# Optimization experiments

Hardware: AMD Instinct MI355X
Metric: run time of the kernel (lower is better)

## Reference

```python
import jax, jax.numpy as jnp
import numpy as np

ALPHA = 1.0 / 10.0  # dt / tau

def setup_inputs() -> dict:
    key = jax.random.key(0)
    ks = jax.random.split(key, 5)
    seq_len, batch, input_dim, hidden = 256, 128, 256, 1024
    return {
        "input": jax.random.normal(ks[0], (seq_len, batch, input_dim), dtype=jnp.float32),
        "W_in": jax.random.normal(ks[1], (hidden, input_dim), dtype=jnp.float32) / np.sqrt(input_dim),
        "b_in": jax.random.normal(ks[2], (hidden,), dtype=jnp.float32) * 0.01,
        "W_hh": jax.random.normal(ks[3], (hidden, hidden), dtype=jnp.float32) / np.sqrt(hidden),
        "b_hh": jax.random.normal(ks[4], (hidden,), dtype=jnp.float32) * 0.01,
        "h0": jnp.zeros((hidden,), dtype=jnp.float32),
    }

def reference(input, W_in, b_in, W_hh, b_hh, h0):
    # input: [T, B, I] -> states: [T, B, H]
    # Precompute input projections for all timesteps (linear, same math as per-step).
    x_proj = jnp.einsum('tbi,hi->tbh', input, W_in) + b_in  # [T, B, H]
    h_init = jnp.broadcast_to(h0, (input.shape[1], h0.shape[0]))  # [B, H]

    def step(h, xp):
        rec = h @ W_hh.T + b_hh                       # [B, H]
        h_new = (1.0 - ALPHA) * h + ALPHA * (rec + xp)  # leaky integration (noise sigma = 0)
        h_new = jax.nn.relu(h_new)
        return h_new, h_new

    _, states = jax.lax.scan(step, h_init, x_proj)
    return states  # [T, B, H]
```

## Files before the change

kernel.cpp:

```cpp
#include <hip/hip_runtime.h>
#include <hip/hip_bf16.h>

#define T_LEN 256
#define B_DIM 128
#define I_DIM 256
#define H_DIM 1024

typedef __attribute__((ext_vector_type(8))) short short8;
typedef __attribute__((ext_vector_type(4))) float f32x4;

__device__ unsigned g_sync[256];

static __device__ __forceinline__ unsigned short f2bf(float f) {
  unsigned u = __float_as_uint(f);
  return (unsigned short)((u + 0x7fffu + ((u >> 16) & 1u)) >> 16);
}
static __device__ __forceinline__ float bf2f(unsigned short h) {
  return __uint_as_float((unsigned)h << 16);
}

__global__ __launch_bounds__(256) void xproj_gemm(
    const float* __restrict__ A, const float* __restrict__ W,
    const float* __restrict__ bias, float* __restrict__ C) {
  __shared__ float As[64][33];
  __shared__ float Ws[64][33];

  const int tid = threadIdx.x;
  const int m0 = blockIdx.y * 64;
  const int n0 = blockIdx.x * 64;
  const int ty = tid >> 4;
  const int tx = tid & 15;
  const int r   = tid >> 3;
  const int c4  = (tid & 7) << 2;

  float acc[4][4] = {};

  for (int kc = 0; kc < I_DIM; kc += 32) {
#pragma unroll
    for (int p = 0; p < 2; ++p) {
      const int rr = r + p * 32;
      const float4 a = *(const float4*)(A + (size_t)(m0 + rr) * I_DIM + kc + c4);
      As[rr][c4 + 0] = a.x; As[rr][c4 + 1] = a.y;
      As[rr][c4 + 2] = a.z; As[rr][c4 + 3] = a.w;
      const float4 w = *(const float4*)(W + (size_t)(n0 + rr) * I_DIM + kc + c4);
      Ws[rr][c4 + 0] = w.x; Ws[rr][c4 + 1] = w.y;
      Ws[rr][c4 + 2] = w.z; Ws[rr][c4 + 3] = w.w;
    }
    __syncthreads();
#pragma unroll
    for (int k = 0; k < 32; ++k) {
      float av[4], wv[4];
#pragma unroll
      for (int i = 0; i < 4; ++i) av[i] = As[ty * 4 + i][k];
#pragma unroll
      for (int j = 0; j < 4; ++j) wv[j] = Ws[tx * 4 + j][k];
#pragma unroll
      for (int i = 0; i < 4; ++i)
#pragma unroll
        for (int j = 0; j < 4; ++j)
          acc[i][j] = fmaf(av[i], wv[j], acc[i][j]);
    }
    __syncthreads();
  }

  const float4 bv = *(const float4*)(bias + n0 + tx * 4);
#pragma unroll
  for (int i = 0; i < 4; ++i) {
    float4 o;
    o.x = acc[i][0] + bv.x;
    o.y = acc[i][1] + bv.y;
    o.z = acc[i][2] + bv.z;
    o.w = acc[i][3] + bv.w;
    *(float4*)(C + (size_t)(m0 + ty * 4 + i) * H_DIM + n0 + tx * 4) = o;
  }
}

__global__ __launch_bounds__(256) void cvt_hi_lo(
    const float* __restrict__ X, unsigned short* __restrict__ Xh,
    unsigned short* __restrict__ Xl) {
  const int i4 = blockIdx.x * 256 + threadIdx.x;
  const float4 x = ((const float4*)X)[i4];
  ushort4 h, l;
  h.x = f2bf(x.x); l.x = f2bf(x.x - bf2f(h.x));
  h.y = f2bf(x.y); l.y = f2bf(x.y - bf2f(h.y));
  h.z = f2bf(x.z); l.z = f2bf(x.z - bf2f(h.z));
  h.w = f2bf(x.w); l.w = f2bf(x.w - bf2f(h.w));
  ((ushort4*)Xh)[i4] = h;
  ((ushort4*)Xl)[i4] = l;
}

__global__ __launch_bounds__(256) void xproj_mfma(
    const unsigned short* __restrict__ Ah, const unsigned short* __restrict__ Al,
    const unsigned short* __restrict__ Wh, const unsigned short* __restrict__ Wl,
    const float* __restrict__ bias, float* __restrict__ C) {
  const int tid  = threadIdx.x;
  const int wv   = tid >> 6;
  const int lane = tid & 63;
  const int ln   = lane & 15;
  const int q    = lane >> 4;
  const int mw   = wv >> 1;
  const int nw   = wv & 1;
  const int m0   = blockIdx.y * 128 + mw * 64;
  const int n0   = blockIdx.x * 64  + nw * 32;

  f32x4 acc[4][2] = {};

#pragma unroll
  for (int kc = 0; kc < 8; ++kc) {
    const int ko = kc * 32 + q * 8;
    short8 afh[4], afl[4], wfh[2], wfl[2];
#pragma unroll
    for (int fm = 0; fm < 4; ++fm) {
      const size_t off = (size_t)(m0 + fm * 16 + ln) * I_DIM + ko;
      afh[fm] = *(const short8*)(Ah + off);
      afl[fm] = *(const short8*)(Al + off);
    }
#pragma unroll
    for (int fn = 0; fn < 2; ++fn) {
      const size_t off = (size_t)(n0 + fn * 16 + ln) * I_DIM + ko;
      wfh[fn] = *(const short8*)(Wh + off);
      wfl[fn] = *(const short8*)(Wl + off);
    }
#pragma unroll
    for (int fm = 0; fm < 4; ++fm)
#pragma unroll
      for (int fn = 0; fn < 2; ++fn) {
        acc[fm][fn] = __builtin_amdgcn_mfma_f32_16x16x32_bf16(afh[fm], wfh[fn], acc[fm][fn], 0, 0, 0);
        acc[fm][fn] = __builtin_amdgcn_mfma_f32_16x16x32_bf16(afh[fm], wfl[fn], acc[fm][fn], 0, 0, 0);
        acc[fm][fn] = __builtin_amdgcn_mfma_f32_16x16x32_bf16(afl[fm], wfh[fn], acc[fm][fn], 0, 0, 0);
      }
  }

#pragma unroll
  for (int fn = 0; fn < 2; ++fn) {
    const int j = n0 + fn * 16 + ln;
    const float bj = bias[j];
#pragma unroll
    for (int fm = 0; fm < 4; ++fm)
#pragma unroll
      for (int r = 0; r < 4; ++r)
        C[(size_t)(m0 + fm * 16 + q * 4 + r) * H_DIM + j] = acc[fm][fn][r] + bj;
  }
}

__global__ __launch_bounds__(256) void cvt_w_bf16(
    const float* __restrict__ W, unsigned short* __restrict__ Wb) {
  const int i4 = blockIdx.x * 256 + threadIdx.x;
  const float4 w = ((const float4*)W)[i4];
  ushort4 o;
  o.x = f2bf(w.x); o.y = f2bf(w.y); o.z = f2bf(w.z); o.w = f2bf(w.w);
  ((ushort4*)Wb)[i4] = o;
}

__global__ __launch_bounds__(256) void init_hT0(
    const float* __restrict__ h0, unsigned short* __restrict__ hT) {
  const int idx = blockIdx.x * 256 + threadIdx.x;
  hT[idx] = f2bf(h0[idx & (H_DIM - 1)]);
  if (blockIdx.x == 0) g_sync[threadIdx.x] = 0u;
}

__global__ __launch_bounds__(256, 1) void rnn_persist(
    unsigned short* __restrict__ hT,
    const unsigned short* __restrict__ Wb,
    const float* __restrict__ b_hh,
    const float* __restrict__ h0,
    float* __restrict__ out)
{
  __shared__ float red[2][16][33];

  const int tid  = threadIdx.x;
  const int wv   = tid >> 6;
  const int lane = tid & 63;
  const int ln   = lane & 15;
  const int q    = lane >> 4;

  const int bid = blockIdx.x;
  const int bq  = bid >> 5;
  const int lj  = bid & 31;
  const int j0  = lj * 32;
  const int mt  = wv & 1;
  const int kh  = wv >> 1;
  const int b0  = bq * 32 + mt * 16;

  short8 wfrag[2][16];
#pragma unroll
  for (int jf = 0; jf < 2; ++jf) {
    const short8* __restrict__ wb8 =
        (const short8*)(Wb + (size_t)(j0 + jf * 16 + ln) * H_DIM + kh * 512 + q * 8);
#pragma unroll
    for (int kc = 0; kc < 16; ++kc) wfrag[jf][kc] = wb8[kc * 4];
  }

  const size_t HT = (size_t)B_DIM * H_DIM;
  const size_t arow = (size_t)(b0 + ln) * H_DIM + kh * 512 + q * 8;
  const unsigned short* __restrict__ ha0 = hT + arow;
  const unsigned short* __restrict__ ha1 = hT + HT + arow;

  float bj[2];
#pragma unroll
  for (int jf = 0; jf < 2; ++jf) bj[jf] = b_hh[j0 + jf * 16 + ln];

  const size_t obase = (size_t)(b0 + q * 4) * H_DIM + j0 + ln;

  float hcur[2][4];
#pragma unroll
  for (int jf = 0; jf < 2; ++jf) {
    const float h0j = h0[j0 + jf * 16 + ln];
#pragma unroll
    for (int r = 0; r < 4; ++r) hcur[jf][r] = h0j;
  }

  unsigned* flags = &g_sync[bq * 32];
  unsigned* myflag = &g_sync[bq * 32 + lj];
  unsigned* pollp  = &g_sync[bq * 32 + kh * 16 + ln];

  for (int t = 0; t < T_LEN; ++t) {
#pragma unroll
    for (int jf = 0; jf < 2; ++jf)
#pragma unroll
      for (int kc = 0; kc < 16; ++kc) asm volatile("" : "+v"(wfrag[jf][kc]));

    float* __restrict__ xio_t = out + (size_t)t * HT;

    float xpv[2][4];
    if (wv < 2) {
#pragma unroll
      for (int jf = 0; jf < 2; ++jf)
#pragma unroll
        for (int r = 0; r < 4; ++r)
          xpv[jf][r] = xio_t[obase + (size_t)r * H_DIM + jf * 16];
    }

    if (t > 0) {
      const unsigned tgt = (unsigned)t;
      for (;;) {
        unsigned fv;
        asm volatile("global_load_dword %0, %1, off sc0 sc1\n\t"
                     "s_waitcnt vmcnt(0)"
                     : "=v"(fv) : "v"(pollp) : "memory");
        if (__all((int)fv >= (int)tgt)) break;
        __builtin_amdgcn_s_sleep(1);
      }
    }
    __builtin_amdgcn_sched_barrier(0);

    const unsigned short* __restrict__ ha = (t & 1) ? ha1 : ha0;
    short8 hfrag[16];
#pragma unroll
    for (int kc = 0; kc < 16; ++kc) {
      asm volatile("global_load_dwordx4 %0, %1, off offset:%2 sc0 sc1"
                   : "=&v"(hfrag[kc]) : "v"(ha), "i"(kc * 64));
    }
    asm volatile("s_waitcnt vmcnt(0)" ::: "memory");
    __builtin_amdgcn_sched_barrier(0);

    f32x4 a0[2], a1[2];
#pragma unroll
    for (int jf = 0; jf < 2; ++jf) { a0[jf] = (f32x4){0,0,0,0}; a1[jf] = (f32x4){0,0,0,0}; }
#pragma unroll
    for (int kc = 0; kc < 16; kc += 2) {
#pragma unroll
      for (int jf = 0; jf < 2; ++jf) {
        a0[jf] = __builtin_amdgcn_mfma_f32_16x16x32_bf16(hfrag[kc],     wfrag[jf][kc],     a0[jf], 0, 0, 0);
        a1[jf] = __builtin_amdgcn_mfma_f32_16x16x32_bf16(hfrag[kc + 1], wfrag[jf][kc + 1], a1[jf], 0, 0, 0);
      }
    }
    f32x4 acc[2];
#pragma unroll
    for (int jf = 0; jf < 2; ++jf) acc[jf] = a0[jf] + a1[jf];

    if (wv >= 2) {
#pragma unroll
      for (int jf = 0; jf < 2; ++jf)
#pragma unroll
        for (int r = 0; r < 4; ++r) red[mt][q * 4 + r][jf * 16 + ln] = acc[jf][r];
    }
    __syncthreads();
    if (wv < 2) {
      unsigned short* __restrict__ hnext = hT + (size_t)((t + 1) & 1) * HT;
#pragma unroll
      for (int jf = 0; jf < 2; ++jf)
#pragma unroll
        for (int r = 0; r < 4; ++r) {
          const float rec = acc[jf][r] + red[mt][q * 4 + r][jf * 16 + ln];
          float v = 0.9f * hcur[jf][r] + 0.1f * (rec + bj[jf] + xpv[jf][r]);
          v = v > 0.f ? v : 0.f;
          hcur[jf][r] = v;
          const size_t oidx = obase + (size_t)r * H_DIM + jf * 16;
          xio_t[oidx] = v;
          __hip_atomic_store(&hnext[oidx], f2bf(v), __ATOMIC_RELAXED,
                             __HIP_MEMORY_SCOPE_AGENT);
        }
    }
    __syncthreads();
    if (tid == 0)
      __hip_atomic_store(myflag, (unsigned)(t + 1), __ATOMIC_RELAXED,
                         __HIP_MEMORY_SCOPE_AGENT);
  }
  (void)flags;
}

extern "C" void kernel_launch(void* const* d_in, const int* in_sizes, int n_in,
                              void* d_out, int out_size, void* d_ws, size_t ws_size,
                              hipStream_t stream) {
  const float* input = (const float*)d_in[0];
  const float* W_in  = (const float*)d_in[1];
  const float* b_in  = (const float*)d_in[2];
  const float* W_hh  = (const float*)d_in[3];
  const float* b_hh  = (const float*)d_in[4];
  const float* h0    = (const float*)d_in[5];
  float* out = (float*)d_out;

  char* ws = (char*)d_ws;
  unsigned short* Wb  = (unsigned short*)ws;
  unsigned short* hT  = (unsigned short*)(ws + (2u << 20));
  unsigned short* Wih = (unsigned short*)(ws + (5u << 19));
  unsigned short* Wil = (unsigned short*)(ws + (3u << 20));
  unsigned short* Ah  = (unsigned short*)(ws + (4u << 20));
  unsigned short* Al  = (unsigned short*)(ws + (20u << 20));

  cvt_w_bf16<<<(H_DIM * H_DIM / 4) / 256, 256, 0, stream>>>(W_hh, Wb);
  init_hT0<<<(B_DIM * H_DIM) / 256, 256, 0, stream>>>(h0, hT);

  if (ws_size >= (36u << 20)) {
    cvt_hi_lo<<<(T_LEN * B_DIM * I_DIM / 4) / 256, 256, 0, stream>>>(input, Ah, Al);
    cvt_hi_lo<<<(H_DIM * I_DIM / 4) / 256, 256, 0, stream>>>(W_in, Wih, Wil);
    dim3 g1(H_DIM / 64, (T_LEN * B_DIM) / 128);
    xproj_mfma<<<g1, 256, 0, stream>>>(Ah, Al, Wih, Wil, b_in, out);
  } else {
    dim3 g1(H_DIM / 64, (T_LEN * B_DIM) / 64);
    xproj_gemm<<<g1, 256, 0, stream>>>(input, W_in, b_in, out);
  }

  {
    unsigned short* hT_ = hT;
    const unsigned short* Wb_ = Wb;
    const float* bhh_ = b_hh;
    const float* h0_ = h0;
    float* out_ = out;
    void* pargs[5] = {(void*)&hT_, (void*)&Wb_, (void*)&bhh_, (void*)&h0_, (void*)&out_};
    hipLaunchCooperativeKernel((const void*)rnn_persist, dim3(128), dim3(256),
                               pargs, 0, stream);
  }
}
```

Baseline: 1.552 ms.

## Move W_hh fragments to LDS, prefetch next x-proj, and per-wave flag signalling

Weight fragments move from VGPRs into shared memory and are read from LDS inside the MFMA loop, which lowers register pressure at the cost of extra LDS traffic every step. The next timestep's input projection is prefetched while the current h loads are in flight. The reduction buffer is double-buffered so the second __syncthreads can be dropped. Each writer wave now publishes its own flag right after its h stores, with the output store moved after the flag, so the next step's dependency is released sooner. The change depends on the relaxed stores and vmcnt waits being enough to order the h writes before the flag.

After: 1.936 ms. +24.7%, slower.

```diff
diff --git a/kernel.cpp b/kernel.cpp
--- a/kernel.cpp
+++ b/kernel.cpp
@@ -166,7 +166,8 @@
     const float* __restrict__ h0,
     float* __restrict__ out)
 {
-  __shared__ float red[2][16][33];
+  __shared__ short8 w_lds[2 * 2 * 16 * 64];
+  __shared__ float red[2][2][16][33];
 
   const int tid  = threadIdx.x;
   const int wv   = tid >> 6;
@@ -182,13 +183,13 @@
   const int kh  = wv >> 1;
   const int b0  = bq * 32 + mt * 16;
 
-  short8 wfrag[2][16];
-#pragma unroll
-  for (int jf = 0; jf < 2; ++jf) {
-    const short8* __restrict__ wb8 =
-        (const short8*)(Wb + (size_t)(j0 + jf * 16 + ln) * H_DIM + kh * 512 + q * 8);
-#pragma unroll
-    for (int kc = 0; kc < 16; ++kc) wfrag[jf][kc] = wb8[kc * 4];
+  {
+    const int kh_f = wv >> 1, jf_f = wv & 1;
+    const short8* __restrict__ src =
+        (const short8*)(Wb + (size_t)(j0 + jf_f * 16 + ln) * H_DIM + kh_f * 512 + q * 8);
+    short8* dst = &w_lds[((kh_f * 2 + jf_f) * 16) * 64 + lane];
+#pragma unroll
+    for (int kc = 0; kc < 16; ++kc) dst[kc * 64] = src[kc * 4];
   }
 
   const size_t HT = (size_t)B_DIM * H_DIM;
@@ -210,27 +211,21 @@
     for (int r = 0; r < 4; ++r) hcur[jf][r] = h0j;
   }
 
-  unsigned* flags = &g_sync[bq * 32];
-  unsigned* myflag = &g_sync[bq * 32 + lj];
-  unsigned* pollp  = &g_sync[bq * 32 + kh * 16 + ln];
+  unsigned* pollp  = &g_sync[bq * 64 + kh * 32 + ((lane & 15) << 1) + mt];
+  unsigned* myflag = &g_sync[bq * 64 + (lj << 1) + mt];
+
+  float xcur[2][4];
+  if (wv < 2) {
+#pragma unroll
+    for (int jf = 0; jf < 2; ++jf)
+#pragma unroll
+      for (int r = 0; r < 4; ++r)
+        xcur[jf][r] = out[obase + (size_t)r * H_DIM + jf * 16];
+  }
+  asm volatile("s_waitcnt vmcnt(0)" ::: "memory");
+  __syncthreads();
 
   for (int t = 0; t < T_LEN; ++t) {
-#pragma unroll
-    for (int jf = 0; jf < 2; ++jf)
-#pragma unroll
-      for (int kc = 0; kc < 16; ++kc) asm volatile("" : "+v"(wfrag[jf][kc]));
-
-    float* __restrict__ xio_t = out + (size_t)t * HT;
-
-    float xpv[2][4];
-    if (wv < 2) {
-#pragma unroll
-      for (int jf = 0; jf < 2; ++jf)
-#pragma unroll
-        for (int r = 0; r < 4; ++r)
-          xpv[jf][r] = xio_t[obase + (size_t)r * H_DIM + jf * 16];
-    }
-
     if (t > 0) {
       const unsigned tgt = (unsigned)t;
       for (;;) {
@@ -239,7 +234,7 @@
                      "s_waitcnt vmcnt(0)"
                      : "=v"(fv) : "v"(pollp) : "memory");
         if (__all((int)fv >= (int)tgt)) break;
-        __builtin_amdgcn_s_sleep(1);
+        __builtin_amdgcn_s_sleep(2);
       }
     }
     __builtin_amdgcn_sched_barrier(0);
@@ -251,7 +246,23 @@
       asm volatile("global_load_dwordx4 %0, %1, off offset:%2 sc0 sc1"
                    : "=&v"(hfrag[kc]) : "v"(ha), "i"(kc * 64));
     }
-    asm volatile("s_waitcnt vmcnt(0)" ::: "memory");
+
+    float xnext[2][4];
+    if (wv < 2) {
+      const int tn = (t + 1 < T_LEN) ? t + 1 : T_LEN - 1;
+      const float* __restrict__ xnp = out + (size_t)tn * HT;
+#pragma unroll
+      for (int jf = 0; jf < 2; ++jf)
+#pragma unroll
+        for (int r = 0; r < 4; ++r) {
+          const float* p = xnp + obase + (size_t)r * H_DIM + jf * 16;
+          asm volatile("global_load_dword %0, %1, off"
+                       : "=&v"(xnext[jf][r]) : "v"(p));
+        }
+      asm volatile("s_waitcnt vmcnt(8)" ::: "memory");
+    } else {
+      asm volatile("s_waitcnt vmcnt(0)" ::: "memory");
+    }
     __builtin_amdgcn_sched_barrier(0);
 
     f32x4 a0[2], a1[2];
@@ -261,8 +272,10 @@
     for (int kc = 0; kc < 16; kc += 2) {
 #pragma unroll
       for (int jf = 0; jf < 2; ++jf) {
-        a0[jf] = __builtin_amdgcn_mfma_f32_16x16x32_bf16(hfrag[kc],     wfrag[jf][kc],     a0[jf], 0, 0, 0);
-        a1[jf] = __builtin_amdgcn_mfma_f32_16x16x32_bf16(hfrag[kc + 1], wfrag[jf][kc + 1], a1[jf], 0, 0, 0);
+        const short8 w0 = w_lds[((kh * 2 + jf) * 16 + kc) * 64 + lane];
+        const short8 w1 = w_lds[((kh * 2 + jf) * 16 + kc + 1) * 64 + lane];
+        a0[jf] = __builtin_amdgcn_mfma_f32_16x16x32_bf16(hfrag[kc],     w0, a0[jf], 0, 0, 0);
+        a1[jf] = __builtin_amdgcn_mfma_f32_16x16x32_bf16(hfrag[kc + 1], w1, a1[jf], 0, 0, 0);
       }
     }
     f32x4 acc[2];
@@ -273,31 +286,42 @@
 #pragma unroll
       for (int jf = 0; jf < 2; ++jf)
 #pragma unroll
-        for (int r = 0; r < 4; ++r) red[mt][q * 4 + r][jf * 16 + ln] = acc[jf][r];
+        for (int r = 0; r < 4; ++r)
+          red[t & 1][mt][q * 4 + r][jf * 16 + ln] = acc[jf][r];
     }
     __syncthreads();
     if (wv < 2) {
       unsigned short* __restrict__ hnext = hT + (size_t)((t + 1) & 1) * HT;
+      float* __restrict__ xio_t = out + (size_t)t * HT;
+      float v[2][4];
 #pragma unroll
       for (int jf = 0; jf < 2; ++jf)
 #pragma unroll
         for (int r = 0; r < 4; ++r) {
-          const float rec = acc[jf][r] + red[mt][q * 4 + r][jf * 16 + ln];
-          float v = 0.9f * hcur[jf][r] + 0.1f * (rec + bj[jf] + xpv[jf][r]);
-          v = v > 0.f ? v : 0.f;
-          hcur[jf][r] = v;
-          const size_t oidx = obase + (size_t)r * H_DIM + jf * 16;
-          xio_t[oidx] = v;
-          __hip_atomic_store(&hnext[oidx], f2bf(v), __ATOMIC_RELAXED,
-                             __HIP_MEMORY_SCOPE_AGENT);
+          const float rec = acc[jf][r] + red[t & 1][mt][q * 4 + r][jf * 16 + ln];
+          float x = 0.9f * hcur[jf][r] + 0.1f * (rec + bj[jf] + xcur[jf][r]);
+          x = x > 0.f ? x : 0.f;
+          v[jf][r] = x;
+          hcur[jf][r] = x;
+          __hip_atomic_store(&hnext[obase + (size_t)r * H_DIM + jf * 16],
+                             f2bf(x), __ATOMIC_RELAXED, __HIP_MEMORY_SCOPE_AGENT);
         }
-    }
-    __syncthreads();
-    if (tid == 0)
-      __hip_atomic_store(myflag, (unsigned)(t + 1), __ATOMIC_RELAXED,
-                         __HIP_MEMORY_SCOPE_AGENT);
-  }
-  (void)flags;
+      asm volatile("s_waitcnt vmcnt(0)" ::: "memory");
+      __builtin_amdgcn_sched_barrier(0);
+      if ((tid & 63) == 0)
+        __hip_atomic_store(myflag, (unsigned)(t + 1), __ATOMIC_RELAXED,
+                           __HIP_MEMORY_SCOPE_AGENT);
+#pragma unroll
+      for (int jf = 0; jf < 2; ++jf)
+#pragma unroll
+        for (int r = 0; r < 4; ++r)
+          xio_t[obase + (size_t)r * H_DIM + jf * 16] = v[jf][r];
+#pragma unroll
+      for (int jf = 0; jf < 2; ++jf)
+#pragma unroll
+        for (int r = 0; r < 4; ++r) xcur[jf][r] = xnext[jf][r];
+    }
+  }
 }
 
 extern "C" void kernel_launch(void* const* d_in, const int* in_sizes, int n_in,
```

## Shrink persistent RNN to 32 blocks with wider column tiles and L2-streamed weights

Applied to the files above, without the earlier changes.

The recurrent persistent kernel moves from 128 blocks of 256 threads to 32 blocks of 512 threads. Each block now covers 128 hidden columns and splits K four ways across warps, reducing partials through shared memory. Weights are no longer held in registers but reloaded from global memory (L2) each step. The flag poll moves to the end of the step and the next x-projection is prefetched in the epilogue, so fewer blocks synchronise and wait latency is hidden. The cost is using far fewer CUs and extra weight traffic per step.

Measured after the change: 5.474 ms. 253% more time.

```diff
diff --git a/kernel.cpp b/kernel.cpp
--- a/kernel.cpp
+++ b/kernel.cpp
@@ -159,14 +159,14 @@
   if (blockIdx.x == 0) g_sync[threadIdx.x] = 0u;
 }
 
-__global__ __launch_bounds__(256, 1) void rnn_persist(
+__global__ __launch_bounds__(512, 1) void rnn_persist(
     unsigned short* __restrict__ hT,
     const unsigned short* __restrict__ Wb,
     const float* __restrict__ b_hh,
     const float* __restrict__ h0,
     float* __restrict__ out)
 {
-  __shared__ float red[2][16][33];
+  __shared__ float red[2][3][16][132];
 
   const int tid  = threadIdx.x;
   const int wv   = tid >> 6;
@@ -175,129 +175,122 @@
   const int q    = lane >> 4;
 
   const int bid = blockIdx.x;
-  const int bq  = bid >> 5;
-  const int lj  = bid & 31;
-  const int j0  = lj * 32;
+  const int bq  = bid >> 3;
+  const int lj  = bid & 7;
+  const int j0  = lj * 128;
   const int mt  = wv & 1;
-  const int kh  = wv >> 1;
+  const int kq  = wv >> 1;
   const int b0  = bq * 32 + mt * 16;
 
-  short8 wfrag[2][16];
-#pragma unroll
-  for (int jf = 0; jf < 2; ++jf) {
-    const short8* __restrict__ wb8 =
-        (const short8*)(Wb + (size_t)(j0 + jf * 16 + ln) * H_DIM + kh * 512 + q * 8);
-#pragma unroll
-    for (int kc = 0; kc < 16; ++kc) wfrag[jf][kc] = wb8[kc * 4];
-  }
-
   const size_t HT = (size_t)B_DIM * H_DIM;
-  const size_t arow = (size_t)(b0 + ln) * H_DIM + kh * 512 + q * 8;
-  const unsigned short* __restrict__ ha0 = hT + arow;
-  const unsigned short* __restrict__ ha1 = hT + HT + arow;
-
-  float bj[2];
-#pragma unroll
-  for (int jf = 0; jf < 2; ++jf) bj[jf] = b_hh[j0 + jf * 16 + ln];
-
-  const size_t obase = (size_t)(b0 + q * 4) * H_DIM + j0 + ln;
-
-  float hcur[2][4];
-#pragma unroll
-  for (int jf = 0; jf < 2; ++jf) {
-    const float h0j = h0[j0 + jf * 16 + ln];
-#pragma unroll
-    for (int r = 0; r < 4; ++r) hcur[jf][r] = h0j;
-  }
-
-  unsigned* flags = &g_sync[bq * 32];
-  unsigned* myflag = &g_sync[bq * 32 + lj];
-  unsigned* pollp  = &g_sync[bq * 32 + kh * 16 + ln];
+  const unsigned short* __restrict__ ha0 =
+      hT + (size_t)(b0 + ln) * H_DIM + kq * 256 + q * 8;
+  const unsigned short* __restrict__ ha1 = ha0 + HT;
+  const unsigned short* __restrict__ wbase0 =
+      Wb + (size_t)(j0 + ln) * H_DIM + kq * 256 + q * 8;
+
+  const bool epi = (kq == 0);
+
+  float bj[8], hcur[8][4], xcur[8][4];
+  if (epi) {
+#pragma unroll
+    for (int jf = 0; jf < 8; ++jf) {
+      bj[jf] = b_hh[j0 + jf * 16 + ln];
+      const float h0j = h0[j0 + jf * 16 + ln];
+#pragma unroll
+      for (int r = 0; r < 4; ++r) {
+        hcur[jf][r] = h0j;
+        xcur[jf][r] = out[(size_t)(b0 + q * 4 + r) * H_DIM + j0 + jf * 16 + ln];
+      }
+    }
+  }
+
+  unsigned* myflag = &g_sync[bq * 16 + lj * 2 + mt];
+  unsigned* pollw  = &g_sync[bq * 16 + ln];
 
   for (int t = 0; t < T_LEN; ++t) {
-#pragma unroll
-    for (int jf = 0; jf < 2; ++jf)
-#pragma unroll
-      for (int kc = 0; kc < 16; ++kc) asm volatile("" : "+v"(wfrag[jf][kc]));
-
-    float* __restrict__ xio_t = out + (size_t)t * HT;
-
-    float xpv[2][4];
-    if (wv < 2) {
-#pragma unroll
-      for (int jf = 0; jf < 2; ++jf)
+    __syncthreads();
+
+    const unsigned short* wb = wbase0;
+    asm volatile("" : "+v"(wb));
+
+    const unsigned short* __restrict__ ha = (t & 1) ? ha1 : ha0;
+    short8 hfrag[8];
+#pragma unroll
+    for (int kc = 0; kc < 8; ++kc) {
+      asm volatile("global_load_dwordx4 %0, %1, off offset:%2 sc0 sc1"
+                   : "=&v"(hfrag[kc]) : "v"(ha), "i"(kc * 64));
+    }
+    asm volatile("s_waitcnt vmcnt(0)" ::: "memory");
+    __builtin_amdgcn_sched_barrier(0);
+
+    f32x4 acc[8];
+#pragma unroll
+    for (int jf = 0; jf < 8; ++jf) acc[jf] = (f32x4){0.f, 0.f, 0.f, 0.f};
+#pragma unroll
+    for (int kc = 0; kc < 8; ++kc) {
+#pragma unroll
+      for (int jf = 0; jf < 8; ++jf) {
+        const short8 wf = *(const short8*)(wb + (size_t)jf * 16 * H_DIM + kc * 32);
+        acc[jf] = __builtin_amdgcn_mfma_f32_16x16x32_bf16(hfrag[kc], wf, acc[jf], 0, 0, 0);
+      }
+    }
+
+    if (!epi) {
+#pragma unroll
+      for (int jf = 0; jf < 8; ++jf)
 #pragma unroll
         for (int r = 0; r < 4; ++r)
-          xpv[jf][r] = xio_t[obase + (size_t)r * H_DIM + jf * 16];
-    }
-
-    if (t > 0) {
-      const unsigned tgt = (unsigned)t;
+          red[mt][kq - 1][q * 4 + r][jf * 16 + ln] = acc[jf][r];
+    }
+    __syncthreads();
+
+    if (epi) {
+      unsigned short* __restrict__ hnext = hT + (size_t)((t + 1) & 1) * HT;
+      float* __restrict__ xio_t = out + (size_t)t * HT;
+      float v[8][4];
+#pragma unroll
+      for (int jf = 0; jf < 8; ++jf)
+#pragma unroll
+        for (int r = 0; r < 4; ++r) {
+          const int jl = jf * 16 + ln;
+          const int bl = q * 4 + r;
+          const float rec = acc[jf][r] + red[mt][0][bl][jl] +
+                            red[mt][1][bl][jl] + red[mt][2][bl][jl];
+          float x = 0.9f * hcur[jf][r] + 0.1f * (rec + bj[jf] + xcur[jf][r]);
+          x = x > 0.f ? x : 0.f;
+          v[jf][r] = x;
+          hcur[jf][r] = x;
+          __hip_atomic_store(&hnext[(size_t)(b0 + bl) * H_DIM + j0 + jl],
+                             f2bf(x), __ATOMIC_RELAXED, __HIP_MEMORY_SCOPE_AGENT);
+        }
+      asm volatile("s_waitcnt vmcnt(0)" ::: "memory");
+      __builtin_amdgcn_sched_barrier(0);
+      if (lane == 0)
+        __hip_atomic_store(myflag, (unsigned)(t + 1), __ATOMIC_RELAXED,
+                           __HIP_MEMORY_SCOPE_AGENT);
+      const int tn = (t + 1 < T_LEN) ? t + 1 : t;
+      const float* __restrict__ xnp = out + (size_t)tn * HT;
+#pragma unroll
+      for (int jf = 0; jf < 8; ++jf)
+#pragma unroll
+        for (int r = 0; r < 4; ++r) {
+          const size_t oidx = (size_t)(b0 + q * 4 + r) * H_DIM + j0 + jf * 16 + ln;
+          xio_t[oidx] = v[jf][r];
+          xcur[jf][r] = xnp[oidx];
+        }
+    } else if (wv == 2 && t + 1 < T_LEN) {
+      const unsigned tgt = (unsigned)(t + 1);
       for (;;) {
         unsigned fv;
         asm volatile("global_load_dword %0, %1, off sc0 sc1\n\t"
                      "s_waitcnt vmcnt(0)"
-                     : "=v"(fv) : "v"(pollp) : "memory");
+                     : "=v"(fv) : "v"(pollw) : "memory");
         if (__all((int)fv >= (int)tgt)) break;
         __builtin_amdgcn_s_sleep(1);
       }
     }
-    __builtin_amdgcn_sched_barrier(0);
-
-    const unsigned short* __restrict__ ha = (t & 1) ? ha1 : ha0;
-    short8 hfrag[16];
-#pragma unroll
-    for (int kc = 0; kc < 16; ++kc) {
-      asm volatile("global_load_dwordx4 %0, %1, off offset:%2 sc0 sc1"
-                   : "=&v"(hfrag[kc]) : "v"(ha), "i"(kc * 64));
-    }
-    asm volatile("s_waitcnt vmcnt(0)" ::: "memory");
-    __builtin_amdgcn_sched_barrier(0);
-
-    f32x4 a0[2], a1[2];
-#pragma unroll
-    for (int jf = 0; jf < 2; ++jf) { a0[jf] = (f32x4){0,0,0,0}; a1[jf] = (f32x4){0,0,0,0}; }
-#pragma unroll
-    for (int kc = 0; kc < 16; kc += 2) {
-#pragma unroll
-      for (int jf = 0; jf < 2; ++jf) {
-        a0[jf] = __builtin_amdgcn_mfma_f32_16x16x32_bf16(hfrag[kc],     wfrag[jf][kc],     a0[jf], 0, 0, 0);
-        a1[jf] = __builtin_amdgcn_mfma_f32_16x16x32_bf16(hfrag[kc + 1], wfrag[jf][kc + 1], a1[jf], 0, 0, 0);
-      }
-    }
-    f32x4 acc[2];
-#pragma unroll
-    for (int jf = 0; jf < 2; ++jf) acc[jf] = a0[jf] + a1[jf];
-
-    if (wv >= 2) {
-#pragma unroll
-      for (int jf = 0; jf < 2; ++jf)
-#pragma unroll
-        for (int r = 0; r < 4; ++r) red[mt][q * 4 + r][jf * 16 + ln] = acc[jf][r];
-    }
-    __syncthreads();
-    if (wv < 2) {
-      unsigned short* __restrict__ hnext = hT + (size_t)((t + 1) & 1) * HT;
-#pragma unroll
-      for (int jf = 0; jf < 2; ++jf)
-#pragma unroll
-        for (int r = 0; r < 4; ++r) {
-          const float rec = acc[jf][r] + red[mt][q * 4 + r][jf * 16 + ln];
-          float v = 0.9f * hcur[jf][r] + 0.1f * (rec + bj[jf] + xpv[jf][r]);
-          v = v > 0.f ? v : 0.f;
-          hcur[jf][r] = v;
-          const size_t oidx = obase + (size_t)r * H_DIM + jf * 16;
-          xio_t[oidx] = v;
-          __hip_atomic_store(&hnext[oidx], f2bf(v), __ATOMIC_RELAXED,
-                             __HIP_MEMORY_SCOPE_AGENT);
-        }
-    }
-    __syncthreads();
-    if (tid == 0)
-      __hip_atomic_store(myflag, (unsigned)(t + 1), __ATOMIC_RELAXED,
-                         __HIP_MEMORY_SCOPE_AGENT);
-  }
-  (void)flags;
+  }
 }
 
 extern "C" void kernel_launch(void* const* d_in, const int* in_sizes, int n_in,
@@ -339,7 +332,7 @@
     const float* h0_ = h0;
     float* out_ = out;
     void* pargs[5] = {(void*)&hT_, (void*)&Wb_, (void*)&bhh_, (void*)&h0_, (void*)&out_};
-    hipLaunchCooperativeKernel((const void*)rnn_persist, dim3(128), dim3(256),
+    hipLaunchCooperativeKernel((const void*)rnn_persist, dim3(32), dim3(512),
                                pargs, 0, stream);
   }
 }
```
